# Performance work log

Hardware: AMD Instinct MI355X
Metric: run time of the kernel (lower is better)

The kernel has to match this reference:

```python
import jax, jax.numpy as jnp
import numpy as np

N = 150000   # nonempty octree nodes at this depth
CIN = 256
CB = 64      # bottleneck channels = out_channels / bottleneck
COUT = 256
G = 32       # group-norm groups
K = 27       # 3x3x3 neighborhood
EPS = 1e-5


def group_norm(x, gamma, beta, groups=G):
    # x: [N, C]; octree GN treats the N nodes as the spatial extent of one instance
    n, c = x.shape
    xg = x.reshape(n, groups, c // groups)
    mu = xg.mean(axis=(0, 2), keepdims=True)
    var = xg.var(axis=(0, 2), keepdims=True)
    xg = (xg - mu) * jax.lax.rsqrt(var + EPS)
    return xg.reshape(n, c) * gamma + beta


def setup_inputs() -> dict:
    key = jax.random.key(0)
    ks = jax.random.split(key, 5)
    return {
        "data": jax.random.normal(ks[0], (N, CIN), jnp.float32),
        "neigh": jax.random.randint(ks[1], (N, K), 0, N, jnp.int32),
        "w1a": jax.random.normal(ks[2], (CIN, CB), jnp.float32) * 0.05,
        "g1a": jnp.ones((CB,), jnp.float32),
        "b1a": jnp.zeros((CB,), jnp.float32),
        "w3": jax.random.normal(ks[3], (K, CB, CB), jnp.float32) * 0.05,
        "g3": jnp.ones((CB,), jnp.float32),
        "b3": jnp.zeros((CB,), jnp.float32),
        "w1b": jax.random.normal(ks[4], (CB, COUT), jnp.float32) * 0.05,
        "g1b": jnp.ones((COUT,), jnp.float32),
        "b1b": jnp.zeros((COUT,), jnp.float32),
    }


def reference(data, neigh, w1a, g1a, b1a, w3, g3, b3, w1b, g1b, b1b):
    # conv1x1a + GN + ReLU
    x = jax.nn.relu(group_norm(data @ w1a, g1a, b1a))
    # octree 3x3x3 sparse conv: gather 27 neighbors, GEMM against [27,CB,CB] kernel
    gathered = x[neigh]                      # [N, 27, CB]
    y = jnp.einsum('nkc,kcd->nd', gathered, w3)
    y = jax.nn.relu(group_norm(y, g3, b3))
    # conv1x1b + GN
    z = group_norm(y @ w1b, g1b, b1b)
    # residual add (in_channels == out_channels -> identity skip) + ReLU
    return jax.nn.relu(z + data)
```

## Files before the change

### kernel.cpp

```cpp
#include <hip/hip_runtime.h>
#include <math.h>

#define CIN 256
#define CB 64
#define COUT 256
#define KNB 27
#define EPS 1e-5f

typedef unsigned short u16;
typedef __attribute__((ext_vector_type(8))) short short8;
typedef __attribute__((ext_vector_type(4))) float f32x4;

__device__ inline short f2bf(float f) {
    union { float f; unsigned u; } v; v.f = f;
    unsigned r = v.u + 0x7fff + ((v.u >> 16) & 1);
    return (short)(r >> 16);
}
__device__ inline float bf2f(short s) {
    union { unsigned u; float f; } v; v.u = ((unsigned)(u16)s) << 16;
    return v.f;
}
__device__ inline short8 pack8(float4 x0, float4 x1) {
    short8 r;
    r[0] = f2bf(x0.x); r[1] = f2bf(x0.y); r[2] = f2bf(x0.z); r[3] = f2bf(x0.w);
    r[4] = f2bf(x1.x); r[5] = f2bf(x1.y); r[6] = f2bf(x1.z); r[7] = f2bf(x1.w);
    return r;
}

__global__ void k_prep(const float* __restrict__ w1a, const float* __restrict__ w3,
                       const float* __restrict__ w1b, u16* __restrict__ w1at,
                       u16* __restrict__ w3img, u16* __restrict__ w1bt)
{
    int i = blockIdx.x * 256 + threadIdx.x;
    if (i < 16384) {
        int k = i >> 6, d = i & 63;
        w1at[d * 256 + k] = (u16)f2bf(w1a[i]);
    } else if (i < 126976) {
        int j = i - 16384;
        int k = j >> 12, c = (j >> 6) & 63, d = j & 63;
        w3img[(size_t)k * 4096 + d * 64 + (c ^ ((d & 7) << 3))] = (u16)f2bf(w3[j]);
    } else if (i < 143360) {
        int j = i - 126976;
        int c = j >> 8, d = j & 255;
        w1bt[d * 64 + c] = (u16)f2bf(w1b[j]);
    }
}

__global__ __launch_bounds__(256) void k_gemm1(const float* __restrict__ data,
        const u16* __restrict__ w1at, u16* __restrict__ t1,
        float* __restrict__ stats, int n)
{
    __shared__ float s_sum[32], s_sq[32];
    const int tid = threadIdx.x;
    if (tid < 32) { s_sum[tid] = 0.f; s_sq[tid] = 0.f; }
    __syncthreads();
    const int l = tid & 63, wv = tid >> 6;
    const int ll = l & 15, lh = l >> 4;
    const int rowbase = blockIdx.x * 256 + wv * 64;

    f32x4 acc[4][4] = {};
#pragma unroll
    for (int kc = 0; kc < 8; ++kc) {
        short8 b[4];
#pragma unroll
        for (int f = 0; f < 4; ++f)
            b[f] = *(const short8*)(w1at + (size_t)(f * 16 + ll) * 256 + kc * 32 + lh * 8);
#pragma unroll
        for (int rt = 0; rt < 4; ++rt) {
            int row = rowbase + rt * 16 + ll;
            int rowc = (row < n) ? row : 0;
            const float* ar = data + (size_t)rowc * CIN + kc * 32 + lh * 8;
            short8 a = pack8(*(const float4*)ar, *(const float4*)(ar + 4));
#pragma unroll
            for (int f = 0; f < 4; ++f)
                acc[rt][f] = __builtin_amdgcn_mfma_f32_16x16x32_bf16(a, b[f], acc[rt][f], 0, 0, 0);
        }
    }
    float gs[4] = {0.f, 0.f, 0.f, 0.f}, gq[4] = {0.f, 0.f, 0.f, 0.f};
#pragma unroll
    for (int rt = 0; rt < 4; ++rt) {
#pragma unroll
        for (int f = 0; f < 4; ++f) {
#pragma unroll
            for (int r = 0; r < 4; ++r) {
                int rr = rowbase + rt * 16 + lh * 4 + r;
                if (rr < n) {
                    float v = acc[rt][f][r];
                    t1[(size_t)rr * CB + f * 16 + ll] = (u16)f2bf(v);
                    gs[f] += v; gq[f] += v * v;
                }
            }
        }
    }
#pragma unroll
    for (int f = 0; f < 4; ++f) {
        float s = gs[f], q = gq[f];
        s += __shfl_xor(s, 1); s += __shfl_xor(s, 16); s += __shfl_xor(s, 32);
        q += __shfl_xor(q, 1); q += __shfl_xor(q, 16); q += __shfl_xor(q, 32);
        if ((l & 0x31) == 0) {
            atomicAdd(&s_sum[f * 8 + (ll >> 1)], s);
            atomicAdd(&s_sq [f * 8 + (ll >> 1)], q);
        }
    }
    __syncthreads();
    if (tid < 32) {
        atomicAdd(&stats[tid], s_sum[tid]);
        atomicAdd(&stats[32 + tid], s_sq[tid]);
    }
}

__global__ void k_apply64(u16* __restrict__ buf, const float* __restrict__ st,
        const float* __restrict__ gamma, const float* __restrict__ beta, int n)
{
    const float cnt = (float)n * 2.0f;
    const int total = n * 8;
    for (int i = blockIdx.x * blockDim.x + threadIdx.x; i < total;
         i += gridDim.x * blockDim.x) {
        int c0 = (i & 7) * 8;
        short8 v = ((short8*)buf)[i];
#pragma unroll
        for (int j = 0; j < 8; ++j) {
            int c = c0 + j, g = c >> 1;
            float mu = st[g] / cnt;
            float var = st[32 + g] / cnt - mu * mu;
            float inv = rsqrtf(var + EPS);
            float x = bf2f(v[j]);
            x = fmaxf((x - mu) * inv * gamma[c] + beta[c], 0.f);
            v[j] = f2bf(x);
        }
        ((short8*)buf)[i] = v;
    }
}

__global__ __launch_bounds__(256, 4) void k_conv(const u16* __restrict__ xb,
        const int* __restrict__ neigh, const u16* __restrict__ w3img,
        u16* __restrict__ y, float* __restrict__ stats, int n)
{
    __shared__ u16 s_w3[2][4096];
    __shared__ int s_idx[128 * KNB];
    __shared__ float s_sum[32], s_sq[32];
    const int tid = threadIdx.x;
    if (tid < 32) { s_sum[tid] = 0.f; s_sq[tid] = 0.f; }
    const int row0 = blockIdx.x * 128;
    for (int j = tid; j < 128 * KNB; j += 256) {
        int node = row0 + j / KNB;
        s_idx[j] = (node < n) ? neigh[(size_t)row0 * KNB + j] : 0;
    }
    const int l = tid & 63, wv = tid >> 6;
    const int ll = l & 15, lh = l >> 4;

    {
        const short8* src = (const short8*)(w3img);
        short8 v0 = src[tid * 2], v1 = src[tid * 2 + 1];
        ((short8*)&s_w3[0][0])[tid * 2] = v0;
        ((short8*)&s_w3[0][0])[tid * 2 + 1] = v1;
    }
    __syncthreads();
    short8 a0c[2], a1c[2];
#pragma unroll
    for (int rt = 0; rt < 2; ++rt) {
        int idx = s_idx[(wv * 32 + rt * 16 + ll) * KNB];
        const u16* xr = xb + (size_t)idx * CB + lh * 8;
        a0c[rt] = *(const short8*)(xr);
        a1c[rt] = *(const short8*)(xr + 32);
    }

    f32x4 acc[2][4] = {};
    for (int k = 0; k < KNB; ++k) {
        const int cur = k & 1;
        const bool more = (k + 1 < KNB);
        short8 w0, w1;
        short8 a0n[2], a1n[2];
        if (more) {
            const short8* src = (const short8*)(w3img + (size_t)(k + 1) * 4096);
            w0 = src[tid * 2];
            w1 = src[tid * 2 + 1];
#pragma unroll
            for (int rt = 0; rt < 2; ++rt) {
                int idx = s_idx[(wv * 32 + rt * 16 + ll) * KNB + k + 1];
                const u16* xr = xb + (size_t)idx * CB + lh * 8;
                a0n[rt] = *(const short8*)(xr);
                a1n[rt] = *(const short8*)(xr + 32);
            }
        }
#pragma unroll
        for (int f = 0; f < 4; ++f) {
            int d = f * 16 + ll;
            int swz = (d & 7) << 4;
            short8 b0 = *(const short8*)((const char*)&s_w3[cur][0] + d * 128 + ((lh * 16) ^ swz));
            short8 b1 = *(const short8*)((const char*)&s_w3[cur][0] + d * 128 + ((64 + lh * 16) ^ swz));
#pragma unroll
            for (int rt = 0; rt < 2; ++rt) {
                acc[rt][f] = __builtin_amdgcn_mfma_f32_16x16x32_bf16(a0c[rt], b0, acc[rt][f], 0, 0, 0);
                acc[rt][f] = __builtin_amdgcn_mfma_f32_16x16x32_bf16(a1c[rt], b1, acc[rt][f], 0, 0, 0);
            }
        }
        if (more) {
            ((short8*)&s_w3[cur ^ 1][0])[tid * 2] = w0;
            ((short8*)&s_w3[cur ^ 1][0])[tid * 2 + 1] = w1;
#pragma unroll
            for (int rt = 0; rt < 2; ++rt) { a0c[rt] = a0n[rt]; a1c[rt] = a1n[rt]; }
        }
        __syncthreads();
    }
    float gs[4] = {0.f, 0.f, 0.f, 0.f}, gq[4] = {0.f, 0.f, 0.f, 0.f};
#pragma unroll
    for (int rt = 0; rt < 2; ++rt) {
#pragma unroll
        for (int f = 0; f < 4; ++f) {
#pragma unroll
            for (int r = 0; r < 4; ++r) {
                int rr = row0 + wv * 32 + rt * 16 + lh * 4 + r;
                if (rr < n) {
                    float v = acc[rt][f][r];
                    y[(size_t)rr * CB + f * 16 + ll] = (u16)f2bf(v);
                    gs[f] += v; gq[f] += v * v;
                }
            }
        }
    }
#pragma unroll
    for (int f = 0; f < 4; ++f) {
        float s = gs[f], q = gq[f];
        s += __shfl_xor(s, 1); s += __shfl_xor(s, 16); s += __shfl_xor(s, 32);
        q += __shfl_xor(q, 1); q += __shfl_xor(q, 16); q += __shfl_xor(q, 32);
        if ((l & 0x31) == 0) {
            atomicAdd(&s_sum[f * 8 + (ll >> 1)], s);
            atomicAdd(&s_sq [f * 8 + (ll >> 1)], q);
        }
    }
    __syncthreads();
    if (tid < 32) {
        atomicAdd(&stats[64 + tid], s_sum[tid]);
        atomicAdd(&stats[96 + tid], s_sq[tid]);
    }
}

__global__ __launch_bounds__(256) void k_gemm2(const u16* __restrict__ y2,
        const u16* __restrict__ w1bt, float* __restrict__ z, u16* __restrict__ zb,
        float* __restrict__ stats, int n)
{
    __shared__ float s_sum[8], s_sq[8];
    const int tid = threadIdx.x;
    if (tid < 8) { s_sum[tid] = 0.f; s_sq[tid] = 0.f; }
    __syncthreads();
    const int l = tid & 63, wv = tid >> 6;
    const int ll = l & 15, lh = l >> 4;
    const int rowbase = blockIdx.x * 256 + wv * 64;
    const int cb = blockIdx.y;

    short8 b0[4], b1[4];
#pragma unroll
    for (int f = 0; f < 4; ++f) {
        const u16* br = w1bt + (size_t)(cb * 64 + f * 16 + ll) * CB + lh * 8;
        b0[f] = *(const short8*)(br);
        b1[f] = *(const short8*)(br + 32);
    }
    f32x4 acc[4][4] = {};
#pragma unroll
    for (int rt = 0; rt < 4; ++rt) {
        int row = rowbase + rt * 16 + ll;
        int rowc = (row < n) ? row : 0;
        const u16* ar = y2 + (size_t)rowc * CB + lh * 8;
        short8 a0 = *(const short8*)(ar);
        short8 a1 = *(const short8*)(ar + 32);
#pragma unroll
        for (int f = 0; f < 4; ++f) {
            acc[rt][f] = __builtin_amdgcn_mfma_f32_16x16x32_bf16(a0, b0[f], acc[rt][f], 0, 0, 0);
            acc[rt][f] = __builtin_amdgcn_mfma_f32_16x16x32_bf16(a1, b1[f], acc[rt][f], 0, 0, 0);
        }
    }
    float gs[4] = {0.f, 0.f, 0.f, 0.f}, gq[4] = {0.f, 0.f, 0.f, 0.f};
#pragma unroll
    for (int rt = 0; rt < 4; ++rt) {
#pragma unroll
        for (int f = 0; f < 4; ++f) {
#pragma unroll
            for (int r = 0; r < 4; ++r) {
                int rr = rowbase + rt * 16 + lh * 4 + r;
                if (rr < n) {
                    float v = acc[rt][f][r];
                    size_t off = (size_t)rr * COUT + cb * 64 + f * 16 + ll;
                    if (zb) zb[off] = (u16)f2bf(v); else z[off] = v;
                    gs[f] += v; gq[f] += v * v;
                }
            }
        }
    }
#pragma unroll
    for (int f = 0; f < 4; ++f) {
        float s = gs[f], q = gq[f];
        s += __shfl_xor(s, 1); s += __shfl_xor(s, 2); s += __shfl_xor(s, 4);
        s += __shfl_xor(s, 16); s += __shfl_xor(s, 32);
        q += __shfl_xor(q, 1); q += __shfl_xor(q, 2); q += __shfl_xor(q, 4);
        q += __shfl_xor(q, 16); q += __shfl_xor(q, 32);
        if ((l & 0x37) == 0) {
            atomicAdd(&s_sum[f * 2 + (ll >> 3)], s);
            atomicAdd(&s_sq [f * 2 + (ll >> 3)], q);
        }
    }
    __syncthreads();
    if (tid < 8) {
        atomicAdd(&stats[128 + cb * 8 + tid], s_sum[tid]);
        atomicAdd(&stats[160 + cb * 8 + tid], s_sq[tid]);
    }
}

__global__ void k_final_bf(float* __restrict__ out, const u16* __restrict__ zb,
        const float* __restrict__ data, const float* __restrict__ st,
        const float* __restrict__ gamma, const float* __restrict__ beta, int n)
{
    const float cnt = (float)n * 8.0f;
    const int total = n * 32;
    for (int i = blockIdx.x * blockDim.x + threadIdx.x; i < total;
         i += gridDim.x * blockDim.x) {
        int c0 = (i & 31) * 8;
        int g = c0 >> 3;
        float mu = st[g] / cnt;
        float var = st[32 + g] / cnt - mu * mu;
        float inv = rsqrtf(var + EPS);
        short8 zv = ((const short8*)zb)[i];
        float dd[8], oo[8];
        *(float4*)dd = *(const float4*)(data + (size_t)i * 8);
        *(float4*)(dd + 4) = *(const float4*)(data + (size_t)i * 8 + 4);
#pragma unroll
        for (int j = 0; j < 8; ++j)
            oo[j] = fmaxf((bf2f(zv[j]) - mu) * inv * gamma[c0 + j] + beta[c0 + j] + dd[j], 0.f);
        *(float4*)(out + (size_t)i * 8) = *(float4*)oo;
        *(float4*)(out + (size_t)i * 8 + 4) = *(float4*)(oo + 4);
    }
}

__global__ void k_final(float* __restrict__ zo, const float* __restrict__ data,
        const float* __restrict__ st, const float* __restrict__ gamma,
        const float* __restrict__ beta, int n)
{
    const float cnt = (float)n * 8.0f;
    const int total = n * (COUT / 4);
    for (int i = blockIdx.x * blockDim.x + threadIdx.x; i < total;
         i += gridDim.x * blockDim.x) {
        int c4 = (i & (COUT / 4 - 1)) * 4;
        int g = c4 >> 3;
        float mu = st[g] / cnt;
        float var = st[32 + g] / cnt - mu * mu;
        float inv = rsqrtf(var + EPS);
        float4 zv = *(float4*)(zo + (size_t)i * 4);
        float4 dv = *(const float4*)(data + (size_t)i * 4);
        zv.x = fmaxf((zv.x - mu) * inv * gamma[c4 + 0] + beta[c4 + 0] + dv.x, 0.f);
        zv.y = fmaxf((zv.y - mu) * inv * gamma[c4 + 1] + beta[c4 + 1] + dv.y, 0.f);
        zv.z = fmaxf((zv.z - mu) * inv * gamma[c4 + 2] + beta[c4 + 2] + dv.z, 0.f);
        zv.w = fmaxf((zv.w - mu) * inv * gamma[c4 + 3] + beta[c4 + 3] + dv.w, 0.f);
        *(float4*)(zo + (size_t)i * 4) = zv;
    }
}

extern "C" void kernel_launch(void* const* d_in, const int* in_sizes, int n_in,
                              void* d_out, int out_size, void* d_ws, size_t ws_size,
                              hipStream_t stream)
{
    const float* data = (const float*)d_in[0];
    const int*   neigh = (const int*)d_in[1];
    const float* w1a = (const float*)d_in[2];
    const float* g1a = (const float*)d_in[3];
    const float* b1a = (const float*)d_in[4];
    const float* w3  = (const float*)d_in[5];
    const float* g3  = (const float*)d_in[6];
    const float* b3  = (const float*)d_in[7];
    const float* w1b = (const float*)d_in[8];
    const float* g1b = (const float*)d_in[9];
    const float* b1b = (const float*)d_in[10];
    float* out = (float*)d_out;
    float* ws  = (float*)d_ws;

    const int n = in_sizes[0] / CIN;

    float* stats = ws;
    u16* w1at  = (u16*)(ws + 256);
    u16* w3img = w1at + 16384;
    u16* w1bt  = w3img + 110592;
    u16* t1    = w1bt + 16384;
    u16* ybuf  = t1 + (size_t)n * CB;
    u16* zb    = nullptr;
    {
        size_t need = 1024 + 286720 + (size_t)n * CB * 4 + (size_t)n * COUT * 2;
        if (ws_size >= need) zb = ybuf + (size_t)n * CB;
    }

    hipMemsetAsync(stats, 0, 192 * sizeof(float), stream);

    const int nb128 = (n + 127) / 128;
    const int nb256 = (n + 255) / 256;
    k_prep<<<560, 256, 0, stream>>>(w1a, w3, w1b, w1at, w3img, w1bt);
    k_gemm1<<<nb256, 256, 0, stream>>>(data, w1at, t1, stats, n);
    k_apply64<<<2048, 256, 0, stream>>>(t1, stats, g1a, b1a, n);
    k_conv<<<nb128, 256, 0, stream>>>(t1, neigh, w3img, ybuf, stats, n);
    k_apply64<<<2048, 256, 0, stream>>>(ybuf, stats + 64, g3, b3, n);
    k_gemm2<<<dim3(nb256, 4), 256, 0, stream>>>(ybuf, w1bt, out, zb, stats, n);
    if (zb)
        k_final_bf<<<2048, 256, 0, stream>>>(out, zb, data, stats + 128, g1b, b1b, n);
    else
        k_final<<<2048, 256, 0, stream>>>(out, data, stats + 128, g1b, b1b, n);
}
```

Baseline: 296.4 us.

## Fuse second GroupNorm+ReLU into gemm2 and shrink conv tile to 64 rows

The conv kernel now processes 64 rows per block, one 16-row tile per wave. It reads neighbor indices directly from global memory with a two-step prefetch instead of staging them in shared memory. The separate normalize-and-ReLU pass over the conv output is removed and applied while loading A operands inside gemm2, which saves one read-write pass over the buffer. Halving the rows per block doubles the number of blocks, so each 27-step weight stream is shared by fewer rows and there are more barriers per row. In return the kernel gets lower register pressure and more blocks to spread across the GPU.

```diff
diff --git a/kernel.cpp b/kernel.cpp
--- a/kernel.cpp
+++ b/kernel.cpp
@@ -132,22 +132,20 @@
     }
 }
 
-__global__ __launch_bounds__(256, 4) void k_conv(const u16* __restrict__ xb,
+__global__ __launch_bounds__(256) void k_conv(const u16* __restrict__ xb,
         const int* __restrict__ neigh, const u16* __restrict__ w3img,
         u16* __restrict__ y, float* __restrict__ stats, int n)
 {
     __shared__ u16 s_w3[2][4096];
-    __shared__ int s_idx[128 * KNB];
     __shared__ float s_sum[32], s_sq[32];
     const int tid = threadIdx.x;
     if (tid < 32) { s_sum[tid] = 0.f; s_sq[tid] = 0.f; }
-    const int row0 = blockIdx.x * 128;
-    for (int j = tid; j < 128 * KNB; j += 256) {
-        int node = row0 + j / KNB;
-        s_idx[j] = (node < n) ? neigh[(size_t)row0 * KNB + j] : 0;
-    }
+    const int row0 = blockIdx.x * 64;
     const int l = tid & 63, wv = tid >> 6;
     const int ll = l & 15, lh = l >> 4;
+    const int myrow = row0 + wv * 16 + ll;
+    const int rowc = (myrow < n) ? myrow : 0;
+    const int* __restrict__ nrow = neigh + (size_t)rowc * KNB;
 
     {
         const short8* src = (const short8*)(w3img);
@@ -155,33 +153,30 @@
         ((short8*)&s_w3[0][0])[tid * 2] = v0;
         ((short8*)&s_w3[0][0])[tid * 2 + 1] = v1;
     }
-    __syncthreads();
-    short8 a0c[2], a1c[2];
-#pragma unroll
-    for (int rt = 0; rt < 2; ++rt) {
-        int idx = s_idx[(wv * 32 + rt * 16 + ll) * KNB];
-        const u16* xr = xb + (size_t)idx * CB + lh * 8;
-        a0c[rt] = *(const short8*)(xr);
-        a1c[rt] = *(const short8*)(xr + 32);
-    }
-
-    f32x4 acc[2][4] = {};
+    int idx0 = nrow[0];
+    int idxn = nrow[1];
+    __syncthreads();
+    short8 a0c, a1c;
+    {
+        const u16* xr = xb + (size_t)idx0 * CB + lh * 8;
+        a0c = *(const short8*)(xr);
+        a1c = *(const short8*)(xr + 32);
+    }
+
+    f32x4 acc[4] = {};
     for (int k = 0; k < KNB; ++k) {
         const int cur = k & 1;
         const bool more = (k + 1 < KNB);
-        short8 w0, w1;
-        short8 a0n[2], a1n[2];
+        int idx2 = 0;
+        short8 w0, w1, a0n, a1n;
+        if (k + 2 < KNB) idx2 = nrow[k + 2];
         if (more) {
             const short8* src = (const short8*)(w3img + (size_t)(k + 1) * 4096);
             w0 = src[tid * 2];
             w1 = src[tid * 2 + 1];
-#pragma unroll
-            for (int rt = 0; rt < 2; ++rt) {
-                int idx = s_idx[(wv * 32 + rt * 16 + ll) * KNB + k + 1];
-                const u16* xr = xb + (size_t)idx * CB + lh * 8;
-                a0n[rt] = *(const short8*)(xr);
-                a1n[rt] = *(const short8*)(xr + 32);
-            }
+            const u16* xr = xb + (size_t)idxn * CB + lh * 8;
+            a0n = *(const short8*)(xr);
+            a1n = *(const short8*)(xr + 32);
         }
 #pragma unroll
         for (int f = 0; f < 4; ++f) {
@@ -189,33 +184,26 @@
             int swz = (d & 7) << 4;
             short8 b0 = *(const short8*)((const char*)&s_w3[cur][0] + d * 128 + ((lh * 16) ^ swz));
             short8 b1 = *(const short8*)((const char*)&s_w3[cur][0] + d * 128 + ((64 + lh * 16) ^ swz));
-#pragma unroll
-            for (int rt = 0; rt < 2; ++rt) {
-                acc[rt][f] = __builtin_amdgcn_mfma_f32_16x16x32_bf16(a0c[rt], b0, acc[rt][f], 0, 0, 0);
-                acc[rt][f] = __builtin_amdgcn_mfma_f32_16x16x32_bf16(a1c[rt], b1, acc[rt][f], 0, 0, 0);
-            }
+            acc[f] = __builtin_amdgcn_mfma_f32_16x16x32_bf16(a0c, b0, acc[f], 0, 0, 0);
+            acc[f] = __builtin_amdgcn_mfma_f32_16x16x32_bf16(a1c, b1, acc[f], 0, 0, 0);
         }
         if (more) {
             ((short8*)&s_w3[cur ^ 1][0])[tid * 2] = w0;
             ((short8*)&s_w3[cur ^ 1][0])[tid * 2 + 1] = w1;
-#pragma unroll
-            for (int rt = 0; rt < 2; ++rt) { a0c[rt] = a0n[rt]; a1c[rt] = a1n[rt]; }
+            a0c = a0n; a1c = a1n; idxn = idx2;
         }
         __syncthreads();
     }
     float gs[4] = {0.f, 0.f, 0.f, 0.f}, gq[4] = {0.f, 0.f, 0.f, 0.f};
 #pragma unroll
-    for (int rt = 0; rt < 2; ++rt) {
-#pragma unroll
-        for (int f = 0; f < 4; ++f) {
-#pragma unroll
-            for (int r = 0; r < 4; ++r) {
-                int rr = row0 + wv * 32 + rt * 16 + lh * 4 + r;
-                if (rr < n) {
-                    float v = acc[rt][f][r];
-                    y[(size_t)rr * CB + f * 16 + ll] = (u16)f2bf(v);
-                    gs[f] += v; gq[f] += v * v;
-                }
+    for (int f = 0; f < 4; ++f) {
+#pragma unroll
+        for (int r = 0; r < 4; ++r) {
+            int rr = row0 + wv * 16 + lh * 4 + r;
+            if (rr < n) {
+                float v = acc[f][r];
+                y[(size_t)rr * CB + f * 16 + ll] = (u16)f2bf(v);
+                gs[f] += v; gq[f] += v * v;
             }
         }
     }
@@ -238,7 +226,8 @@
 
 __global__ __launch_bounds__(256) void k_gemm2(const u16* __restrict__ y2,
         const u16* __restrict__ w1bt, float* __restrict__ z, u16* __restrict__ zb,
-        float* __restrict__ stats, int n)
+        float* __restrict__ stats, const float* __restrict__ g3,
+        const float* __restrict__ b3, int n)
 {
     __shared__ float s_sum[8], s_sq[8];
     const int tid = threadIdx.x;
@@ -249,6 +238,21 @@
     const int rowbase = blockIdx.x * 256 + wv * 64;
     const int cb = blockIdx.y;
 
+    const float* st2 = stats + 64;
+    const float cnt2 = (float)n * 2.0f;
+    float sc[16], sh[16];
+#pragma unroll
+    for (int j = 0; j < 16; ++j) {
+        int c = (j < 8) ? (lh * 8 + j) : (32 + lh * 8 + (j - 8));
+        int g = c >> 1;
+        float mu = st2[g] / cnt2;
+        float var = st2[32 + g] / cnt2 - mu * mu;
+        float inv = rsqrtf(var + EPS);
+        float gm = g3[c];
+        sc[j] = inv * gm;
+        sh[j] = b3[c] - mu * inv * gm;
+    }
+
     short8 b0[4], b1[4];
 #pragma unroll
     for (int f = 0; f < 4; ++f) {
@@ -262,8 +266,14 @@
         int row = rowbase + rt * 16 + ll;
         int rowc = (row < n) ? row : 0;
         const u16* ar = y2 + (size_t)rowc * CB + lh * 8;
-        short8 a0 = *(const short8*)(ar);
-        short8 a1 = *(const short8*)(ar + 32);
+        short8 r0 = *(const short8*)(ar);
+        short8 r1 = *(const short8*)(ar + 32);
+        short8 a0, a1;
+#pragma unroll
+        for (int j = 0; j < 8; ++j) {
+            a0[j] = f2bf(fmaxf(bf2f(r0[j]) * sc[j] + sh[j], 0.f));
+            a1[j] = f2bf(fmaxf(bf2f(r1[j]) * sc[8 + j] + sh[8 + j], 0.f));
+        }
 #pragma unroll
         for (int f = 0; f < 4; ++f) {
             acc[rt][f] = __builtin_amdgcn_mfma_f32_16x16x32_bf16(a0, b0[f], acc[rt][f], 0, 0, 0);
@@ -388,14 +398,13 @@
 
     hipMemsetAsync(stats, 0, 192 * sizeof(float), stream);
 
-    const int nb128 = (n + 127) / 128;
+    const int nb64  = (n + 63) / 64;
     const int nb256 = (n + 255) / 256;
     k_prep<<<560, 256, 0, stream>>>(w1a, w3, w1b, w1at, w3img, w1bt);
     k_gemm1<<<nb256, 256, 0, stream>>>(data, w1at, t1, stats, n);
     k_apply64<<<2048, 256, 0, stream>>>(t1, stats, g1a, b1a, n);
-    k_conv<<<nb128, 256, 0, stream>>>(t1, neigh, w3img, ybuf, stats, n);
-    k_apply64<<<2048, 256, 0, stream>>>(ybuf, stats + 64, g3, b3, n);
-    k_gemm2<<<dim3(nb256, 4), 256, 0, stream>>>(ybuf, w1bt, out, zb, stats, n);
+    k_conv<<<nb64, 256, 0, stream>>>(t1, neigh, w3img, ybuf, stats, n);
+    k_gemm2<<<dim3(nb256, 4), 256, 0, stream>>>(ybuf, w1bt, out, zb, stats, g3, b3, n);
     if (zb)
         k_final_bf<<<2048, 256, 0, stream>>>(out, zb, data, stats + 128, g1b, b1b, n);
     else
```

Result: no change. 296.1 us (-0.1%).
